# Kernel optimization log

Hardware: AMD Instinct MI355X
Metric: run time of the kernel (lower is better)

Reference implementation:

```python
import jax, jax.numpy as jnp
import numpy as np

N_NODES = 100000
N_EDGES = 1600000
D_IN = 128
D_OUT = 128


def setup_inputs() -> dict:
    key = jax.random.key(0)
    k1, k2, k3, k4 = jax.random.split(key, 4)
    x = jax.random.normal(k1, (N_NODES, D_IN), dtype=jnp.float32)
    edge_index = jax.random.randint(k2, (2, N_EDGES), 0, N_NODES, dtype=jnp.int64)
    # Xavier-uniform init as in the torch module
    limit = float(np.sqrt(6.0 / (D_IN + D_OUT)))
    self_weight = jax.random.uniform(k3, (D_IN, D_OUT), dtype=jnp.float32, minval=-limit, maxval=limit)
    neighbor_weight = jax.random.uniform(k4, (D_IN, D_OUT), dtype=jnp.float32, minval=-limit, maxval=limit)
    bias = jnp.zeros((D_OUT,), dtype=jnp.float32)
    return {"x": x, "edge_index": edge_index, "self_weight": self_weight,
            "neighbor_weight": neighbor_weight, "bias": bias}


def reference(x, edge_index, self_weight, neighbor_weight, bias):
    row, col = edge_index[0], edge_index[1]
    num_nodes = x.shape[0]
    # symmetric normalization: deg^-1/2 over rows, gathered per edge
    deg = jax.ops.segment_sum(jnp.ones_like(row, dtype=x.dtype), row,
                              num_segments=num_nodes)
    deg_inv_sqrt = deg ** -0.5
    norm = deg_inv_sqrt[row] * deg_inv_sqrt[col]  # [E]
    # dense transforms
    self_support = x @ self_weight                 # [N, D_OUT]
    h = x @ neighbor_weight                        # [N, D_OUT]
    # spmm: out[r] += norm_e * h[c] for each edge (r, c)
    msg = norm[:, None] * h[col]                   # [E, D_OUT]
    neighbor_support = jax.ops.segment_sum(msg, row, num_segments=num_nodes)
    return self_support + neighbor_support + bias
```

## Files before the change

kernel.cpp:

```cpp
#include <hip/hip_runtime.h>

#define N_NODES 100000
#define N_EDGES 1600000
#define D_FEAT 128
#define BUCKETS 512
#define RPB 196
#define BKCAP 4096
#define BIN_CHUNK 8192
#define BIN_WGS ((N_EDGES + BIN_CHUNK - 1) / BIN_CHUNK)

#define CONV_ELEMS (N_NODES * D_FEAT / 4)
#define CONV_WGS 2048
#define WPREP_WGS 16
#define PREB_WGS (BIN_WGS + WPREP_WGS + CONV_WGS)

typedef unsigned int u32;
typedef unsigned short u16;
typedef __attribute__((ext_vector_type(8))) short bf16x8;
typedef __attribute__((ext_vector_type(4))) float f32x4;

__device__ inline float bfbits2f(u32 hi) { union { u32 u; float f; } v; v.u = hi; return v.f; }
__device__ inline float bflo(u32 pair) { return bfbits2f(pair << 16); }
__device__ inline float bfhi(u32 pair) { return bfbits2f(pair & 0xFFFF0000u); }
__device__ inline u16 f2bf(float f) {
  union { float f; u32 u; } v; v.f = f;
  u32 r = v.u + 0x7FFFu + ((v.u >> 16) & 1u);
  return (u16)(r >> 16);
}
__device__ inline int clampN(int v) { return ((unsigned)v < N_NODES) ? v : 0; }

__global__ __launch_bounds__(256) void k_preb(const int* __restrict__ ei,
                                              int* __restrict__ gcur,
                                              u32* __restrict__ binrec,
                                              const float4* __restrict__ x4,
                                              uint2* __restrict__ xb2,
                                              const float* __restrict__ Wself,
                                              const float* __restrict__ Wnb,
                                              u16* __restrict__ Wbf) {
  __shared__ int hist[BUCKETS], pref[BUCKETS], lcur[BUCKETS], ps[256];
  __shared__ u32 stag[BIN_CHUNK];
  __shared__ u16 sbkt[BIN_CHUNK];
  int b = blockIdx.x;
  int tid = threadIdx.x;
  if (b >= BIN_WGS + WPREP_WGS) {
    int cb = b - BIN_WGS - WPREP_WGS;
    for (int i = cb * 256 + tid; i < CONV_ELEMS; i += CONV_WGS * 256) {
      float4 v = x4[i];
      uint2 o;
      o.x = (u32)f2bf(v.x) | ((u32)f2bf(v.y) << 16);
      o.y = (u32)f2bf(v.z) | ((u32)f2bf(v.w) << 16);
      xb2[i] = o;
    }
    return;
  }
  if (b >= BIN_WGS) {
    int f = (b - BIN_WGS) * 256 + tid;
    int lane = f & 63, nt = (f >> 6) & 7, kk = (f >> 9) & 3, t = f >> 11;
    int q = lane >> 4, l16 = lane & 15;
    const float* W = t ? Wnb : Wself;
    int n = nt * 16 + l16;
    int k0 = (kk * 4 + q) * 8;
    u16 tmp[8];
#pragma unroll
    for (int j = 0; j < 8; j++) tmp[j] = f2bf(W[(k0 + j) * 128 + n]);
    uint4 o;
    o.x = (u32)tmp[0] | ((u32)tmp[1] << 16);
    o.y = (u32)tmp[2] | ((u32)tmp[3] << 16);
    o.z = (u32)tmp[4] | ((u32)tmp[5] << 16);
    o.w = (u32)tmp[6] | ((u32)tmp[7] << 16);
    *(uint4*)(Wbf + (long)f * 8) = o;
    return;
  }
  long e0 = (long)b * BIN_CHUNK;
  for (int k = tid; k < BUCKETS; k += 256) { hist[k] = 0; lcur[k] = 0; }
  __syncthreads();
  int rows[BIN_CHUNK / 256];
#pragma unroll
  for (int j = 0; j < BIN_CHUNK / 256; j++) {
    long e = e0 + j * 256 + tid;
    int r = (e < N_EDGES) ? clampN(ei[e]) : -1;
    rows[j] = r;
    if (r >= 0) atomicAdd(&hist[r / RPB], 1);
  }
  __syncthreads();
  int v0 = hist[2 * tid], v1 = hist[2 * tid + 1];
  int s = v0 + v1;
  ps[tid] = s;
  __syncthreads();
  for (int off = 1; off < 256; off <<= 1) {
    int t = (tid >= off) ? ps[tid - off] : 0;
    __syncthreads();
    ps[tid] += t;
    __syncthreads();
  }
  int excl = ps[tid] - s;
  pref[2 * tid] = excl;
  pref[2 * tid + 1] = excl + v0;
  hist[2 * tid] = (2 * tid) * BKCAP + (v0 ? atomicAdd(&gcur[2 * tid], v0) : 0);
  hist[2 * tid + 1] = (2 * tid + 1) * BKCAP + (v1 ? atomicAdd(&gcur[2 * tid + 1], v1) : 0);
  int total = ps[255];
  __syncthreads();
#pragma unroll
  for (int j = 0; j < BIN_CHUNK / 256; j++) {
    int r = rows[j];
    if (r < 0) continue;
    long e = e0 + j * 256 + tid;
    int c = clampN(ei[N_EDGES + e]);
    int bk = r / RPB;
    int rl = r - bk * RPB;
    int pos = pref[bk] + atomicAdd(&lcur[bk], 1);
    stag[pos] = ((u32)rl << 17) | (u32)c;
    sbkt[pos] = (u16)bk;
  }
  __syncthreads();
  for (int i = tid; i < total; i += 256) {
    int bk = sbkt[i];
    int idx = hist[bk] + (i - pref[bk]);
    if (idx < (bk + 1) * BKCAP) binrec[idx] = stag[i];
  }
}

__global__ __launch_bounds__(256) void k_csr(const int* __restrict__ gcur,
                                             const u32* __restrict__ binrec,
                                             int* __restrict__ deg,
                                             int* __restrict__ row_start,
                                             float* __restrict__ dis,
                                             int* __restrict__ cn) {
  __shared__ int h[256];
  __shared__ int cur[256];
  __shared__ int win[BKCAP];
  int tid = threadIdx.x;
  int b = blockIdx.x;
  int r0 = b * RPB;
  int nrows = N_NODES - r0; if (nrows > RPB) nrows = RPB; if (nrows < 0) nrows = 0;
  int base = b * BKCAP;
  int cnt = gcur[b]; if (cnt > BKCAP) cnt = BKCAP;
  h[tid] = 0;
  __syncthreads();
  for (int i = tid; i < cnt; i += 256) {
    u32 rec = binrec[base + i];
    atomicAdd(&h[rec >> 17], 1);
  }
  __syncthreads();
  int v = h[tid];
  __syncthreads();
  for (int off = 1; off < 256; off <<= 1) {
    int t = (tid >= off) ? h[tid - off] : 0;
    __syncthreads();
    h[tid] += t;
    __syncthreads();
  }
  int excl = h[tid] - v;
  cur[tid] = excl;
  if (tid < nrows) {
    int r = r0 + tid;
    deg[r] = v;
    row_start[r] = base + excl;
    dis[r] = v ? rsqrtf((float)v) : 0.0f;
  }
  __syncthreads();
  for (int i = tid; i < cnt; i += 256) {
    u32 rec = binrec[base + i];
    int rl = rec >> 17;
    int p = atomicAdd(&cur[rl], 1);
    win[p] = (int)(rec & 0x1FFFF);
  }
  __syncthreads();
  for (int i = tid; i < cnt; i += 256) cn[base + i] = win[i];
}

__global__ __launch_bounds__(256) void k_agg(const int* __restrict__ row_start,
                                             const int* __restrict__ deg,
                                             const float* __restrict__ dis,
                                             const int* __restrict__ cn,
                                             const u32* __restrict__ xb ,
                                             u32* __restrict__ aggb) {
  int wave = threadIdx.x >> 6, lane = threadIdx.x & 63;
  int r = blockIdx.x * 4 + wave;
  if (r >= N_NODES) return;
  int start = row_start[r];
  int cnt = deg[r];
  float dr = dis[r];
  float a0 = 0.f, a1 = 0.f, b0 = 0.f, b1 = 0.f;
  int i = 0;
  for (; i + 8 <= cnt; i += 8) {
    int c[8];
    u32 g[8];
    float nc[8];
#pragma unroll
    for (int j = 0; j < 8; j++) c[j] = cn[start + i + j];
#pragma unroll
    for (int j = 0; j < 8; j++) g[j] = xb[(long)c[j] * 64 + lane];
#pragma unroll
    for (int j = 0; j < 8; j++) nc[j] = dis[c[j]];
#pragma unroll
    for (int j = 0; j < 8; j++) {
      float n = dr * nc[j];
      if (j & 1) { b0 += n * bflo(g[j]); b1 += n * bfhi(g[j]); }
      else       { a0 += n * bflo(g[j]); a1 += n * bfhi(g[j]); }
    }
  }
  for (; i + 2 <= cnt; i += 2) {
    int c0 = cn[start + i], c1 = cn[start + i + 1];
    u32 g0 = xb[(long)c0 * 64 + lane];
    u32 g1 = xb[(long)c1 * 64 + lane];
    float n0 = dr * dis[c0], n1 = dr * dis[c1];
    a0 += n0 * bflo(g0); a1 += n0 * bfhi(g0);
    b0 += n1 * bflo(g1); b1 += n1 * bfhi(g1);
  }
  if (i < cnt) {
    int c0 = cn[start + i];
    u32 g0 = xb[(long)c0 * 64 + lane];
    float n0 = dr * dis[c0];
    a0 += n0 * bflo(g0); a1 += n0 * bfhi(g0);
  }
  a0 += b0; a1 += b1;
  aggb[(long)r * 64 + lane] = (u32)f2bf(a0) | ((u32)f2bf(a1) << 16);
}

__global__ __launch_bounds__(256) void k_gemm(const u16* __restrict__ xb,
                                              const u16* __restrict__ aggb,
                                              const u16* __restrict__ Wbf,
                                              const float* __restrict__ bias,
                                              float* __restrict__ out) {
  int tid = threadIdx.x;
  int wave = tid >> 6, lane = tid & 63;
  int q = lane >> 4, l16 = lane & 15;
  int w0 = blockIdx.x * 128 + wave * 32;

  bf16x8 ax[2][4], ag[2][4];
#pragma unroll
  for (int mt = 0; mt < 2; mt++) {
    int node = w0 + mt * 16 + l16;
    long aoff = (long)clampN(node) * D_FEAT + q * 8;
#pragma unroll
    for (int kk = 0; kk < 4; kk++) {
      ax[mt][kk] = *(const bf16x8*)(xb + aoff + kk * 32);
      ag[mt][kk] = *(const bf16x8*)(aggb + aoff + kk * 32);
    }
  }

#pragma unroll
  for (int nt = 0; nt < 8; nt++) {
    bf16x8 bs[4], bn[4];
#pragma unroll
    for (int kk = 0; kk < 4; kk++) {
      bs[kk] = *(const bf16x8*)(Wbf + (long)(((0 * 4 + kk) * 8 + nt) * 64 + lane) * 8);
      bn[kk] = *(const bf16x8*)(Wbf + (long)(((1 * 4 + kk) * 8 + nt) * 64 + lane) * 8);
    }
    int ncol = nt * 16 + l16;
    float bv = bias[ncol];
#pragma unroll
    for (int mt = 0; mt < 2; mt++) {
      f32x4 acc = {0.f, 0.f, 0.f, 0.f};
#pragma unroll
      for (int kk = 0; kk < 4; kk++)
        acc = __builtin_amdgcn_mfma_f32_16x16x32_bf16(ax[mt][kk], bs[kk], acc, 0, 0, 0);
#pragma unroll
      for (int kk = 0; kk < 4; kk++)
        acc = __builtin_amdgcn_mfma_f32_16x16x32_bf16(ag[mt][kk], bn[kk], acc, 0, 0, 0);
#pragma unroll
      for (int reg = 0; reg < 4; reg++) {
        int node = w0 + mt * 16 + q * 4 + reg;
        if (node < N_NODES) out[(long)node * D_FEAT + ncol] = acc[reg] + bv;
      }
    }
  }
}

extern "C" void kernel_launch(void* const* d_in, const int* in_sizes, int n_in,
                              void* d_out, int out_size, void* d_ws, size_t ws_size,
                              hipStream_t stream) {
  const float* x = (const float*)d_in[0];
  const int* ei = (const int*)d_in[1];
  const float* Wself = (const float*)d_in[2];
  const float* Wnb = (const float*)d_in[3];
  const float* bias = (const float*)d_in[4];
  float* out = (float*)d_out;

  auto alignup = [](size_t v) { return (v + 511) & ~(size_t)511; };
  char* p = (char*)d_ws;
  int* deg = (int*)p;            p += alignup((size_t)N_NODES * 4);
  int* row_start = (int*)p;      p += alignup((size_t)N_NODES * 4);
  float* dis = (float*)p;        p += alignup((size_t)N_NODES * 4);
  int* gcur = (int*)p;           p += alignup((size_t)BUCKETS * 4);
  u16* Wbf = (u16*)p;            p += alignup((size_t)4096 * 8 * 2);
  int* cn = (int*)p;             p += alignup((size_t)BUCKETS * BKCAP * 4);
  u16* xb = (u16*)p;             p += alignup((size_t)N_NODES * D_FEAT * 2);
  u16* aggb = (u16*)p;           p += alignup((size_t)N_NODES * D_FEAT * 2);
  u32* binrec = (u32*)d_out;

  hipMemsetAsync(gcur, 0, (size_t)BUCKETS * 4, stream);

  k_preb<<<PREB_WGS, 256, 0, stream>>>(ei, gcur, binrec, (const float4*)x, (uint2*)xb,
                                       Wself, Wnb, Wbf);
  k_csr<<<BUCKETS, 256, 0, stream>>>(gcur, binrec, deg, row_start, dis, cn);
  k_agg<<<(N_NODES + 3) / 4, 256, 0, stream>>>(row_start, deg, dis, cn, (const u32*)xb, (u32*)aggb);
  k_gemm<<<(N_NODES + 127) / 128, 256, 0, stream>>>(xb, aggb, Wbf, bias, out);
}
```

Baseline: 236.4 us.

## Merge memset, binning and CSR build into one cooperative kernel with grid syncs

Replaces the memset, the binning/convert kernel and the CSR kernel with a single cooperative launch of 512 workgroups. Grid-wide syncs separate the gcur reset, the binning/weight-prep/x-convert phase and the per-bucket CSR phase, and shared memory is reused through a union. This removes two launches and the memset, but the x conversion now runs on far fewer workgroups, and grid.sync adds its own cost.

```diff
diff --git a/kernel.cpp b/kernel.cpp
--- a/kernel.cpp
+++ b/kernel.cpp
@@ -1,4 +1,7 @@
 #include <hip/hip_runtime.h>
+#include <hip/hip_cooperative_groups.h>
+
+namespace cg = cooperative_groups;
 
 #define N_NODES 100000
 #define N_EDGES 1600000
@@ -8,11 +11,10 @@
 #define BKCAP 4096
 #define BIN_CHUNK 8192
 #define BIN_WGS ((N_EDGES + BIN_CHUNK - 1) / BIN_CHUNK)
-
+#define WPREP_WGS 16
+#define FRONT_WGS 512
+#define CONV_BLKS (FRONT_WGS - BIN_WGS - WPREP_WGS)
 #define CONV_ELEMS (N_NODES * D_FEAT / 4)
-#define CONV_WGS 2048
-#define WPREP_WGS 16
-#define PREB_WGS (BIN_WGS + WPREP_WGS + CONV_WGS)
 
 typedef unsigned int u32;
 typedef unsigned short u16;
@@ -29,31 +31,81 @@
 }
 __device__ inline int clampN(int v) { return ((unsigned)v < N_NODES) ? v : 0; }
 
-__global__ __launch_bounds__(256) void k_preb(const int* __restrict__ ei,
-                                              int* __restrict__ gcur,
-                                              u32* __restrict__ binrec,
-                                              const float4* __restrict__ x4,
-                                              uint2* __restrict__ xb2,
-                                              const float* __restrict__ Wself,
-                                              const float* __restrict__ Wnb,
-                                              u16* __restrict__ Wbf) {
-  __shared__ int hist[BUCKETS], pref[BUCKETS], lcur[BUCKETS], ps[256];
-  __shared__ u32 stag[BIN_CHUNK];
-  __shared__ u16 sbkt[BIN_CHUNK];
+__global__ __launch_bounds__(256) void k_front(const int* __restrict__ ei,
+                                               int* __restrict__ gcur,
+                                               u32* __restrict__ binrec,
+                                               const float4* __restrict__ x4,
+                                               uint2* __restrict__ xb2,
+                                               const float* __restrict__ Wself,
+                                               const float* __restrict__ Wnb,
+                                               u16* __restrict__ Wbf,
+                                               int* __restrict__ deg,
+                                               int* __restrict__ row_start,
+                                               float* __restrict__ dis,
+                                               int* __restrict__ cn) {
+  __shared__ union {
+    struct { int hist[BUCKETS], pref[BUCKETS], lcur[BUCKETS], ps[256];
+             u32 stag[BIN_CHUNK]; u16 sbkt[BIN_CHUNK]; } bin;
+    struct { int h[256], cur[256], win[BKCAP]; } csr;
+  } sm;
+  cg::grid_group grid = cg::this_grid();
   int b = blockIdx.x;
   int tid = threadIdx.x;
-  if (b >= BIN_WGS + WPREP_WGS) {
-    int cb = b - BIN_WGS - WPREP_WGS;
-    for (int i = cb * 256 + tid; i < CONV_ELEMS; i += CONV_WGS * 256) {
-      float4 v = x4[i];
-      uint2 o;
-      o.x = (u32)f2bf(v.x) | ((u32)f2bf(v.y) << 16);
-      o.y = (u32)f2bf(v.z) | ((u32)f2bf(v.w) << 16);
-      xb2[i] = o;
-    }
-    return;
-  }
-  if (b >= BIN_WGS) {
+
+  if (b == 0) {
+    for (int k = tid; k < BUCKETS; k += 256) gcur[k] = 0;
+  }
+  grid.sync();
+
+  if (b < BIN_WGS) {
+    long e0 = (long)b * BIN_CHUNK;
+    for (int k = tid; k < BUCKETS; k += 256) { sm.bin.hist[k] = 0; sm.bin.lcur[k] = 0; }
+    __syncthreads();
+    int rows[BIN_CHUNK / 256];
+#pragma unroll
+    for (int j = 0; j < BIN_CHUNK / 256; j++) {
+      long e = e0 + j * 256 + tid;
+      int r = (e < N_EDGES) ? clampN(ei[e]) : -1;
+      rows[j] = r;
+      if (r >= 0) atomicAdd(&sm.bin.hist[r / RPB], 1);
+    }
+    __syncthreads();
+    int v0 = sm.bin.hist[2 * tid], v1 = sm.bin.hist[2 * tid + 1];
+    int s = v0 + v1;
+    sm.bin.ps[tid] = s;
+    __syncthreads();
+    for (int off = 1; off < 256; off <<= 1) {
+      int t = (tid >= off) ? sm.bin.ps[tid - off] : 0;
+      __syncthreads();
+      sm.bin.ps[tid] += t;
+      __syncthreads();
+    }
+    int excl = sm.bin.ps[tid] - s;
+    sm.bin.pref[2 * tid] = excl;
+    sm.bin.pref[2 * tid + 1] = excl + v0;
+    sm.bin.hist[2 * tid] = (2 * tid) * BKCAP + (v0 ? atomicAdd(&gcur[2 * tid], v0) : 0);
+    sm.bin.hist[2 * tid + 1] = (2 * tid + 1) * BKCAP + (v1 ? atomicAdd(&gcur[2 * tid + 1], v1) : 0);
+    int total = sm.bin.ps[255];
+    __syncthreads();
+#pragma unroll
+    for (int j = 0; j < BIN_CHUNK / 256; j++) {
+      int r = rows[j];
+      if (r < 0) continue;
+      long e = e0 + j * 256 + tid;
+      int c = clampN(ei[N_EDGES + e]);
+      int bk = r / RPB;
+      int rl = r - bk * RPB;
+      int pos = sm.bin.pref[bk] + atomicAdd(&sm.bin.lcur[bk], 1);
+      sm.bin.stag[pos] = ((u32)rl << 17) | (u32)c;
+      sm.bin.sbkt[pos] = (u16)bk;
+    }
+    __syncthreads();
+    for (int i = tid; i < total; i += 256) {
+      int bk = sm.bin.sbkt[i];
+      int idx = sm.bin.hist[bk] + (i - sm.bin.pref[bk]);
+      if (idx < (bk + 1) * BKCAP) binrec[idx] = sm.bin.stag[i];
+    }
+  } else if (b < BIN_WGS + WPREP_WGS) {
     int f = (b - BIN_WGS) * 256 + tid;
     int lane = f & 63, nt = (f >> 6) & 7, kk = (f >> 9) & 3, t = f >> 11;
     int q = lane >> 4, l16 = lane & 15;
@@ -69,104 +121,56 @@
     o.z = (u32)tmp[4] | ((u32)tmp[5] << 16);
     o.w = (u32)tmp[6] | ((u32)tmp[7] << 16);
     *(uint4*)(Wbf + (long)f * 8) = o;
-    return;
-  }
-  long e0 = (long)b * BIN_CHUNK;
-  for (int k = tid; k < BUCKETS; k += 256) { hist[k] = 0; lcur[k] = 0; }
-  __syncthreads();
-  int rows[BIN_CHUNK / 256];
-#pragma unroll
-  for (int j = 0; j < BIN_CHUNK / 256; j++) {
-    long e = e0 + j * 256 + tid;
-    int r = (e < N_EDGES) ? clampN(ei[e]) : -1;
-    rows[j] = r;
-    if (r >= 0) atomicAdd(&hist[r / RPB], 1);
-  }
-  __syncthreads();
-  int v0 = hist[2 * tid], v1 = hist[2 * tid + 1];
-  int s = v0 + v1;
-  ps[tid] = s;
-  __syncthreads();
-  for (int off = 1; off < 256; off <<= 1) {
-    int t = (tid >= off) ? ps[tid - off] : 0;
-    __syncthreads();
-    ps[tid] += t;
-    __syncthreads();
-  }
-  int excl = ps[tid] - s;
-  pref[2 * tid] = excl;
-  pref[2 * tid + 1] = excl + v0;
-  hist[2 * tid] = (2 * tid) * BKCAP + (v0 ? atomicAdd(&gcur[2 * tid], v0) : 0);
-  hist[2 * tid + 1] = (2 * tid + 1) * BKCAP + (v1 ? atomicAdd(&gcur[2 * tid + 1], v1) : 0);
-  int total = ps[255];
-  __syncthreads();
-#pragma unroll
-  for (int j = 0; j < BIN_CHUNK / 256; j++) {
-    int r = rows[j];
-    if (r < 0) continue;
-    long e = e0 + j * 256 + tid;
-    int c = clampN(ei[N_EDGES + e]);
-    int bk = r / RPB;
-    int rl = r - bk * RPB;
-    int pos = pref[bk] + atomicAdd(&lcur[bk], 1);
-    stag[pos] = ((u32)rl << 17) | (u32)c;
-    sbkt[pos] = (u16)bk;
-  }
-  __syncthreads();
-  for (int i = tid; i < total; i += 256) {
-    int bk = sbkt[i];
-    int idx = hist[bk] + (i - pref[bk]);
-    if (idx < (bk + 1) * BKCAP) binrec[idx] = stag[i];
-  }
-}
-
-__global__ __launch_bounds__(256) void k_csr(const int* __restrict__ gcur,
-                                             const u32* __restrict__ binrec,
-                                             int* __restrict__ deg,
-                                             int* __restrict__ row_start,
-                                             float* __restrict__ dis,
-                                             int* __restrict__ cn) {
-  __shared__ int h[256];
-  __shared__ int cur[256];
-  __shared__ int win[BKCAP];
-  int tid = threadIdx.x;
-  int b = blockIdx.x;
-  int r0 = b * RPB;
-  int nrows = N_NODES - r0; if (nrows > RPB) nrows = RPB; if (nrows < 0) nrows = 0;
-  int base = b * BKCAP;
-  int cnt = gcur[b]; if (cnt > BKCAP) cnt = BKCAP;
-  h[tid] = 0;
-  __syncthreads();
-  for (int i = tid; i < cnt; i += 256) {
-    u32 rec = binrec[base + i];
-    atomicAdd(&h[rec >> 17], 1);
-  }
-  __syncthreads();
-  int v = h[tid];
-  __syncthreads();
-  for (int off = 1; off < 256; off <<= 1) {
-    int t = (tid >= off) ? h[tid - off] : 0;
-    __syncthreads();
-    h[tid] += t;
-    __syncthreads();
-  }
-  int excl = h[tid] - v;
-  cur[tid] = excl;
-  if (tid < nrows) {
-    int r = r0 + tid;
-    deg[r] = v;
-    row_start[r] = base + excl;
-    dis[r] = v ? rsqrtf((float)v) : 0.0f;
-  }
-  __syncthreads();
-  for (int i = tid; i < cnt; i += 256) {
-    u32 rec = binrec[base + i];
-    int rl = rec >> 17;
-    int p = atomicAdd(&cur[rl], 1);
-    win[p] = (int)(rec & 0x1FFFF);
-  }
-  __syncthreads();
-  for (int i = tid; i < cnt; i += 256) cn[base + i] = win[i];
+  } else {
+    int cb = b - BIN_WGS - WPREP_WGS;
+    for (int i = cb * 256 + tid; i < CONV_ELEMS; i += CONV_BLKS * 256) {
+      float4 v = x4[i];
+      uint2 o;
+      o.x = (u32)f2bf(v.x) | ((u32)f2bf(v.y) << 16);
+      o.y = (u32)f2bf(v.z) | ((u32)f2bf(v.w) << 16);
+      xb2[i] = o;
+    }
+  }
+  grid.sync();
+
+  {
+    int r0 = b * RPB;
+    int nrows = N_NODES - r0; if (nrows > RPB) nrows = RPB; if (nrows < 0) nrows = 0;
+    int base = b * BKCAP;
+    int cnt = gcur[b]; if (cnt > BKCAP) cnt = BKCAP;
+    sm.csr.h[tid] = 0;
+    __syncthreads();
+    for (int i = tid; i < cnt; i += 256) {
+      u32 rec = binrec[base + i];
+      atomicAdd(&sm.csr.h[rec >> 17], 1);
+    }
+    __syncthreads();
+    int v = sm.csr.h[tid];
+    __syncthreads();
+    for (int off = 1; off < 256; off <<= 1) {
+      int t = (tid >= off) ? sm.csr.h[tid - off] : 0;
+      __syncthreads();
+      sm.csr.h[tid] += t;
+      __syncthreads();
+    }
+    int excl = sm.csr.h[tid] - v;
+    sm.csr.cur[tid] = excl;
+    if (tid < nrows) {
+      int r = r0 + tid;
+      deg[r] = v;
+      row_start[r] = base + excl;
+      dis[r] = v ? rsqrtf((float)v) : 0.0f;
+    }
+    __syncthreads();
+    for (int i = tid; i < cnt; i += 256) {
+      u32 rec = binrec[base + i];
+      int rl = rec >> 17;
+      int p = atomicAdd(&sm.csr.cur[rl], 1);
+      sm.csr.win[p] = (int)(rec & 0x1FFFF);
+    }
+    __syncthreads();
+    for (int i = tid; i < cnt; i += 256) cn[base + i] = sm.csr.win[i];
+  }
 }
 
 __global__ __launch_bounds__(256) void k_agg(const int* __restrict__ row_start,
@@ -290,11 +294,13 @@
   u16* aggb = (u16*)p;           p += alignup((size_t)N_NODES * D_FEAT * 2);
   u32* binrec = (u32*)d_out;
 
-  hipMemsetAsync(gcur, 0, (size_t)BUCKETS * 4, stream);
-
-  k_preb<<<PREB_WGS, 256, 0, stream>>>(ei, gcur, binrec, (const float4*)x, (uint2*)xb,
-                                       Wself, Wnb, Wbf);
-  k_csr<<<BUCKETS, 256, 0, stream>>>(gcur, binrec, deg, row_start, dis, cn);
+  const float4* x4 = (const float4*)x;
+  uint2* xb2 = (uint2*)xb;
+  void* args[] = {(void*)&ei, (void*)&gcur, (void*)&binrec, (void*)&x4, (void*)&xb2,
+                  (void*)&Wself, (void*)&Wnb, (void*)&Wbf,
+                  (void*)&deg, (void*)&row_start, (void*)&dis, (void*)&cn};
+  hipLaunchCooperativeKernel((void*)k_front, dim3(FRONT_WGS), dim3(256), args, 0, stream);
+
   k_agg<<<(N_NODES + 3) / 4, 256, 0, stream>>>(row_start, deg, dis, cn, (const u32*)xb, (u32*)aggb);
   k_gemm<<<(N_NODES + 127) / 128, 256, 0, stream>>>(xb, aggb, Wbf, bias, out);
 }
```

Measured after the change: 345.5 us. 46.1% more time.
